# Performance work log

Hardware: AMD Instinct MI355X
Metric: run time of the kernel (lower is better)

Reference implementation:

```python
import jax, jax.numpy as jnp
from jax import lax
import numpy as np

KSIZE = 3
STRIDE = 1
PAD = 1
SOFTMAX_SCALE = 10.0
EPS = 1e-4


def _unfold(x, k, stride, pad):
    # x: [B, C, H, W] -> ([B, L, C, k, k], Ho, Wo)  (matches torch nn.Unfold ordering)
    B, C, H, W = x.shape
    xp = jnp.pad(x, ((0, 0), (0, 0), (pad, pad), (pad, pad)))
    Ho = (H + 2 * pad - k) // stride + 1
    Wo = (W + 2 * pad - k) // stride + 1
    cols = jnp.stack(
        [xp[:, :, i:i + Ho * stride:stride, j:j + Wo * stride:stride]
         for i in range(k) for j in range(k)], axis=2)  # [B, C, k*k, Ho, Wo]
    cols = cols.reshape(B, C, k, k, Ho * Wo)
    return cols.transpose(0, 4, 1, 2, 3), Ho, Wo


def setup_inputs() -> dict:
    key = jax.random.key(0)
    kb, kf, km = jax.random.split(key, 3)
    b = jax.random.normal(kb, (4, 64, 64, 64), dtype=jnp.float32)
    f = jax.random.normal(kf, (4, 64, 64, 64), dtype=jnp.float32)
    mask = jax.random.uniform(km, (4, 1, 256, 256), dtype=jnp.float32)
    return {"b": b, "f": f, "mask": mask}


def reference(b, f, mask):
    B, C, H, W = f.shape
    k = KSIZE
    # background patches: [B, L, C, k, k]
    bp, _, _ = _unfold(b, k, STRIDE, PAD)
    # mask: avg_pool2d(kernel=4, stride=mask_scale) with mask_scale = mask.W // f.W = 4
    mp = mask.reshape(B, 1, H, 4, W, 4).mean(axis=(3, 5))  # [B, 1, H, W]
    m_unf, _, _ = _unfold(mp, k, STRIDE, PAD)  # [B, L, 1, k, k]
    m0 = m_unf[0]  # quirk of original code: first sample's mask patches used for all
    w = bp * m0[None]  # masked background patches [B, L, C, k, k]
    f_masked = f * (1.0 - mp)
    # L2 norm over (C, k, k) per patch
    norm = jnp.sqrt(jnp.sum(w * w, axis=(2, 3, 4), keepdims=True) + EPS)
    wn = w / norm
    # cosine-similarity score: conv2d(f_masked, wn) as a GEMM over unfolded f
    fp, Ho, Wo = _unfold(f_masked, k, STRIDE, PAD)  # [B, Q, C, k, k]
    score = jnp.einsum('bqcij,blcij->blq', fp, wn).reshape(B, -1, Ho, Wo)  # [B, L, Ho, Wo]
    attn = jax.nn.softmax(score * SOFTMAX_SCALE, axis=1)
    offsets = jnp.argmax(score, axis=1)[:, None]  # [B, 1, Ho, Wo]
    # conv_transpose2d(attn, w, padding=1) == conv2d with spatially flipped, channel-swapped kernel
    pad_ct = k - 1 - 1

    def _ct(a, w_i):  # a: [L, Ho, Wo], w_i: [L, C, k, k]
        kern = jnp.flip(w_i, axis=(-2, -1)).transpose(1, 0, 2, 3)  # [C, L, k, k]
        return lax.conv_general_dilated(
            a[None], kern, (1, 1), [(pad_ct, pad_ct), (pad_ct, pad_ct)],
            dimension_numbers=('NCHW', 'OIHW', 'NCHW'))[0]

    y = jax.vmap(_ct)(attn, w)  # [B, C, Ho, Wo]
    return y, offsets
```

## Files before the change

### kernel.cpp

```cpp
#include <hip/hip_runtime.h>
#include <math.h>

typedef unsigned int u32;
typedef unsigned short u16;
typedef unsigned long long u64;
typedef _Float16 h8v __attribute__((ext_vector_type(8)));
typedef float f4v __attribute__((ext_vector_type(4)));
typedef u32 u4v __attribute__((ext_vector_type(4)));

#define B_ 4
#define C_ 64
#define HW 4096
#define L_ 4096
#define D_ 576
#define MW 256
#define SCALE 10.0f
#define EPS 1e-4f
#define TAU 0.015f
#define PAIRCAP 262144

__device__ __forceinline__ u16 f16b(float x) {
  union { _Float16 h; u16 u; } c; c.h = (_Float16)x; return c.u;
}
__device__ __forceinline__ float f16f(u16 v) {
  union { u16 u; _Float16 h; } c; c.u = v; return (float)c.h;
}

__device__ __forceinline__ void gld16(const void* g, void* l) {
  __builtin_amdgcn_global_load_lds((const __attribute__((address_space(1))) void*)g,
                                   (__attribute__((address_space(3))) void*)l, 16, 0, 0);
}

__global__ __launch_bounds__(256) void k_mp(const float* __restrict__ mask, float* __restrict__ mp) {
  int idx = blockIdx.x * 256 + threadIdx.x;
  int b = idx >> 12, p = idx & 4095;
  int y = p >> 6, x = p & 63;
  const float* mb = mask + (size_t)b * MW * MW;
  float s = 0.f;
  #pragma unroll
  for (int i = 0; i < 4; ++i)
    #pragma unroll
    for (int j = 0; j < 4; ++j)
      s += mb[(y * 4 + i) * MW + x * 4 + j];
  mp[idx] = s * (1.f / 16.f);
}

__global__ __launch_bounds__(256) void k_pre2(const float* __restrict__ f, const float* __restrict__ mp,
                                              float* __restrict__ m0, float* __restrict__ fm) {
  int blk = blockIdx.x;
  if (blk < 144) {
    int idx = blk * 256 + threadIdx.x;
    int l = idx / 9, t = idx - l * 9;
    int ly = l >> 6, lx = l & 63;
    int i = t / 3, j = t - i * 3;
    int yy = ly + i - 1, xx = lx + j - 1;
    float v = 0.f;
    if ((unsigned)yy < 64u && (unsigned)xx < 64u) v = mp[(yy << 6) + xx];
    m0[idx] = v;
  } else {
    int idx = (blk - 144) * 256 + threadIdx.x;
    int p = idx & 4095;
    int b = idx >> 18;
    fm[idx] = f[idx] * (1.f - mp[(b << 12) + p]);
  }
}

__device__ __forceinline__ float ldsval(const float* __restrict__ s, int lloc, int c, int t) {
  int i2 = t / 3, j2 = t - i2 * 3;
  int xx = lloc + j2 - 1;
  float v = 0.f;
  if ((unsigned)xx < 64u) v = s[(((i2 << 6) + c) << 6) + xx];
  return v;
}

__global__ __launch_bounds__(512) void k_prepw(const float* __restrict__ bimg, const float* __restrict__ fmb,
                                               const float* __restrict__ m0,
                                               u16* __restrict__ w_h, u16* __restrict__ fp_h,
                                               u16* __restrict__ wT_h,
                                               double* __restrict__ norme, float* __restrict__ normv,
                                               int* __restrict__ rcount, int* __restrict__ pcount,
                                               u64* __restrict__ rbest) {
  if (blockIdx.x >= 64) {
    int e = (blockIdx.x - 64) * 512 + threadIdx.x;
    if (e < 4096) rbest[e] = 0ull;
    if (e == 0) { *rcount = 0; *pcount = 0; }
    return;
  }
  __shared__ float s_img[12288];
  __shared__ float s_fm[12288];
  __shared__ float m0s[576];
  const int ly = blockIdx.x;
  const int tid = threadIdx.x;

  #pragma unroll
  for (int i = 0; i < 6; ++i) {
    int slot = tid + i * 512;
    int dy = slot >> 10, rem = slot & 1023;
    int c = rem >> 4, xq = rem & 15;
    int yy = ly + dy - 1;
    f4v vi = {0.f, 0.f, 0.f, 0.f}, vf = {0.f, 0.f, 0.f, 0.f};
    if ((unsigned)yy < 64u) {
      vi = *(const f4v*)&bimg[(c << 12) + (yy << 6) + (xq << 2)];
      vf = *(const f4v*)&fmb[(c << 12) + (yy << 6) + (xq << 2)];
    }
    *(f4v*)&s_img[slot << 2] = vi;
    *(f4v*)&s_fm[slot << 2] = vf;
  }
  for (int t2 = tid; t2 < 576; t2 += 512) m0s[t2] = m0[ly * 576 + t2];
  __syncthreads();

  u32* wh32 = (u32*)w_h;
  u32* fp32p = (u32*)fp_h;
  #pragma unroll
  for (int i = 0; i < 36; ++i) {
    int g2 = tid + i * 512;
    int idx = g2 * 2;
    int ll = idx / 576, d0 = idx - ll * 576;
    int c0 = d0 / 9, t0 = d0 - c0 * 9;
    int d1 = d0 + 1;
    int c1 = d1 / 9, t1 = d1 - c1 * 9;
    float w0 = ldsval(s_img, ll, c0, t0) * m0s[ll * 9 + t0];
    float w1 = ldsval(s_img, ll, c1, t1) * m0s[ll * 9 + t1];
    wh32[ly * 18432 + g2] = (u32)f16b(w0) | ((u32)f16b(w1) << 16);
    float p0 = ldsval(s_fm, ll, c0, t0);
    float p1 = ldsval(s_fm, ll, c1, t1);
    fp32p[ly * 18432 + g2] = (u32)f16b(p0) | ((u32)f16b(p1) << 16);
  }

  u32* wT32 = (u32*)wT_h;
  #pragma unroll
  for (int i = 0; i < 36; ++i) {
    int g2 = tid + i * 512;
    int d = g2 >> 5, lxp = g2 & 31;
    int c = d / 9, t = d - c * 9;
    float w0 = ldsval(s_img, 2 * lxp, c, t) * m0s[(2 * lxp) * 9 + t];
    float w1 = ldsval(s_img, 2 * lxp + 1, c, t) * m0s[(2 * lxp + 1) * 9 + t];
    wT32[d * 2048 + ly * 32 + lxp] = (u32)f16b(w0) | ((u32)f16b(w1) << 16);
  }

  int wid = tid >> 6, lane = tid & 63;
  #pragma unroll
  for (int it = 0; it < 8; ++it) {
    int lloc = wid * 8 + it;
    double ss = 0.0;
    #pragma unroll
    for (int k = 0; k < 9; ++k) {
      int d = lane + k * 64;
      int c = d / 9, t = d - c * 9;
      float wv = ldsval(s_img, lloc, c, t) * m0s[lloc * 9 + t];
      ss += (double)wv * (double)wv;
    }
    #pragma unroll
    for (int off = 32; off; off >>= 1) ss += __shfl_down(ss, off);
    if (lane == 0) {
      double n = sqrt(ss + (double)EPS);
      norme[ly * 64 + lloc] = n;
      normv[ly * 64 + lloc] = (float)n;
    }
  }
}

#define STAGE1(buf, k0) do {                                                             \
    int bb = (buf) * 24576;                                                              \
    _Pragma("unroll") for (int i_ = 0; i_ < 4; ++i_) {                                   \
      int s_ = tid + i_ * 256; int r_ = s_ >> 2, ks_ = s_ & 3;                           \
      int kg_ = ks_ ^ ((r_ >> 1) & 3);                                                   \
      gld16(A + (u32)(m0 + r_) * 576u + (u32)((k0) + kg_ * 8),                           \
            (char*)lds + bb + s_ * 16); }                                                \
    _Pragma("unroll") for (int i_ = 0; i_ < 2; ++i_) {                                   \
      int s_ = tid + i_ * 256; int r_ = s_ >> 2, ks_ = s_ & 3;                           \
      int kg_ = ks_ ^ ((r_ >> 1) & 3);                                                   \
      gld16(Bm + (u32)(n0 + r_) * 576u + (u32)((k0) + kg_ * 8),                          \
            (char*)lds + bb + 16384 + s_ * 16); }                                        \
  } while (0)

__global__ __launch_bounds__(256, 2) void k_mfma1(
    const u16* __restrict__ A, const u16* __restrict__ Bm, const float* __restrict__ normv,
    u16* __restrict__ P, float* __restrict__ bm1, int* __restrict__ bi1,
    float* __restrict__ bsum, int* __restrict__ bflg)
{
  __shared__ u32 lds[18432];
  u16* ldsu = (u16*)lds;
  const int tid = threadIdx.x;
  const int lane = tid & 63, wid = tid >> 6;
  const int wrM = wid >> 1, wc = wid & 1;
  const int kq = lane >> 4, li = lane & 15;

  int nwg = gridDim.x * gridDim.y;
  int bid = blockIdx.y * gridDim.x + blockIdx.x;
  int cpx = nwg >> 3;
  int swz = (bid & 7) * cpx + (bid >> 3);
  int bx = swz % gridDim.x, by = swz / gridDim.x;
  const int m0 = by * 256, n0 = bx * 128;

  f4v acc[8][4] = {};

  STAGE1(0, 0);
  STAGE1(1, 32);

  for (int kc = 0; kc < 18; ++kc) {
    if (kc + 1 < 18) { asm volatile("s_waitcnt vmcnt(6)" ::: "memory"); }
    else             { asm volatile("s_waitcnt vmcnt(0)" ::: "memory"); }
    __builtin_amdgcn_s_barrier();
    __builtin_amdgcn_sched_barrier(0);
    if (kc + 2 < 18) STAGE1((kc + 2) % 3, (kc + 2) * 32);

    int cb = (kc % 3) * 12288;
    h8v ah[8];
    #pragma unroll
    for (int mf = 0; mf < 8; ++mf) {
      int r = wrM * 128 + mf * 16 + li;
      int off = r * 32 + (kq ^ ((r >> 1) & 3)) * 8;
      ah[mf] = *(const h8v*)&ldsu[cb + off];
    }
    #pragma unroll
    for (int nf = 0; nf < 4; ++nf) {
      int r = wc * 64 + nf * 16 + li;
      int off = r * 32 + (kq ^ ((r >> 1) & 3)) * 8;
      h8v bh = *(const h8v*)&ldsu[cb + 8192 + off];
      #pragma unroll
      for (int mf = 0; mf < 8; ++mf)
        acc[mf][nf] = __builtin_amdgcn_mfma_f32_16x16x32_f16(ah[mf], bh, acc[mf][nf], 0, 0, 0);
    }
  }
  __syncthreads();

  float* ldsf = (float*)lds;
  int*   ldsi = (int*)lds;

  float invn4[4];
  #pragma unroll
  for (int nf = 0; nf < 4; ++nf) invn4[nf] = 1.0f / normv[n0 + wc * 64 + nf * 16 + li];
  #pragma unroll
  for (int mf = 0; mf < 8; ++mf)
    #pragma unroll
    for (int nf = 0; nf < 4; ++nf)
      #pragma unroll
      for (int rr = 0; rr < 4; ++rr)
        acc[mf][nf][rr] *= invn4[nf];

  #pragma unroll
  for (int mf = 0; mf < 8; ++mf)
    #pragma unroll
    for (int rr = 0; rr < 4; ++rr) {
      int row = wrM * 128 + mf * 16 + kq * 4 + rr;
      float tv = fmaxf(fmaxf(acc[mf][0][rr], acc[mf][1][rr]), fmaxf(acc[mf][2][rr], acc[mf][3][rr]));
      ldsf[row * 33 + wc * 16 + li] = tv;
    }
  __syncthreads();
  float rV1 = -3.4e38f;
  #pragma unroll
  for (int k = 0; k < 32; ++k) rV1 = fmaxf(rV1, ldsf[tid * 33 + k]);
  ldsf[8448 + tid] = rV1;
  ldsi[8704 + tid] = 0x7fffffff;
  ldsi[8960 + tid] = 0;
  __syncthreads();

  #pragma unroll
  for (int mf = 0; mf < 8; ++mf)
    #pragma unroll
    for (int rr = 0; rr < 4; ++rr) {
      int row = wrM * 128 + mf * 16 + kq * 4 + rr;
      float v1 = ldsf[8448 + row];
      int m = m0 + row;
      float sum4 = 0.f;
      int locmin = 0x7fffffff, loccnt = 0;
      #pragma unroll
      for (int nf = 0; nf < 4; ++nf) {
        float sv = acc[mf][nf][rr];
        int n = n0 + wc * 64 + nf * 16 + li;
        float p = __expf((sv - v1) * SCALE);
        P[(u32)m * 4096u + (u32)n] = f16b(p);
        sum4 += p;
        if (sv == v1 && n < locmin) locmin = n;
        if (sv >= v1 - TAU) loccnt++;
      }
      ldsf[row * 33 + wc * 16 + li] = sum4;
      if (locmin != 0x7fffffff) atomicMin(&ldsi[8704 + row], locmin);
      if (loccnt) atomicAdd(&ldsi[8960 + row], loccnt);
    }
  __syncthreads();

  {
    float rS = 0.f;
    #pragma unroll
    for (int k = 0; k < 32; ++k) rS += ldsf[tid * 33 + k];
    int q = m0 + tid, j = n0 >> 7;
    bm1[q * 32 + j] = ldsf[8448 + tid];
    bi1[q * 32 + j] = ldsi[8704 + tid];
    bsum[q * 32 + j] = rS;
    bflg[q * 32 + j] = (ldsi[8960 + tid] >= 2) ? 1 : 0;
  }
}

__global__ __launch_bounds__(256) void k_smred(const float* __restrict__ bm1, const int* __restrict__ bi1,
                                               const float* __restrict__ bsum, const int* __restrict__ bflg,
                                               float* __restrict__ fac, float* __restrict__ gm,
                                               float* __restrict__ offs, int* __restrict__ rflag,
                                               int* __restrict__ rlist, int* __restrict__ rcount) {
  int q = blockIdx.x * 4 + (threadIdx.x >> 6);
  int lane = threadIdx.x & 63;
  if (lane >= 32) return;
  float mj = bm1[q * 32 + lane];
  int   fj = bflg[q * 32 + lane];
  float v1 = mj; int i1 = bi1[q * 32 + lane];
  #pragma unroll
  for (int d = 1; d < 32; d <<= 1) {
    float ov1 = __shfl_xor(v1, d); int oi1 = __shfl_xor(i1, d);
    if (ov1 > v1 || (ov1 == v1 && oi1 < i1)) { v1 = ov1; i1 = oi1; }
  }
  float e = __expf((mj - v1) * SCALE);
  float Z = bsum[q * 32 + lane] * e;
  #pragma unroll
  for (int d = 1; d < 32; d <<= 1) Z += __shfl_xor(Z, d);
  fac[q * 32 + lane] = e / Z;
  int jwin = i1 >> 7;
  int near = (lane != jwin) && (mj >= v1 - TAU);
  u64 bal = __ballot(near);
  int wflg = __shfl(fj, jwin);
  if (lane == 0) {
    gm[q] = v1;
    offs[q] = (float)i1;
    int fl = (bal != 0ull || wflg) ? 1 : 0;
    rflag[q] = fl;
    if (fl) {
      int pos = atomicAdd(rcount, 1);
      if (pos < 4096) rlist[pos] = q;
    }
  }
}

__global__ __launch_bounds__(256) void k_attnc(u16* __restrict__ P, const float* __restrict__ fac,
                                               const int* __restrict__ rflag, const float* __restrict__ bm1,
                                               const float* __restrict__ gm,
                                               u32* __restrict__ pairs, int* __restrict__ pcount) {
  int gid = blockIdx.x * 256 + threadIdx.x;
  u4v v = ((u4v*)P)[gid];
  int q = gid >> 9;
  int l0 = (gid & 511) * 8;
  int j = l0 >> 7;

  if (rflag[q]) {
    float thr = gm[q] - 2.0f * TAU - 1e-3f;
    float bmj = bm1[q * 32 + j];
    if (bmj >= thr) {
      u16 bits = f16b(__expf((thr - bmj) * SCALE));
      u16 pt = bits > 4 ? (u16)(bits - 4) : (u16)1;
      #pragma unroll
      for (int k = 0; k < 4; ++k) {
        u16 lo = (u16)v[k], hi = (u16)(v[k] >> 16);
        if (lo >= pt) {
          int pos = atomicAdd(pcount, 1);
          if (pos < PAIRCAP) pairs[pos] = ((u32)q << 12) | (u32)(l0 + 2 * k);
        }
        if (hi >= pt) {
          int pos = atomicAdd(pcount, 1);
          if (pos < PAIRCAP) pairs[pos] = ((u32)q << 12) | (u32)(l0 + 2 * k + 1);
        }
      }
    }
  }

  _Float16 fh = (_Float16)fac[q * 32 + j];
  union { u4v u; h8v h; } c; c.u = v;
  c.h *= (h8v){fh, fh, fh, fh, fh, fh, fh, fh};
  ((u4v*)P)[gid] = c.u;
}

#define STG2(buf, k0) do {                                                               \
    int bb = (buf) * 24576;                                                              \
    _Pragma("unroll") for (int i_ = 0; i_ < 4; ++i_) {                                   \
      int s_ = tid + i_ * 256; int r_ = s_ >> 2, ks_ = s_ & 3;                           \
      int kg_ = ks_ ^ ((r_ >> 1) & 3);                                                   \
      gld16(A + (u32)(m0 + r_) * 4096u + (u32)((k0) + kg_ * 8),                          \
            (char*)lds + bb + s_ * 16); }                                                \
    _Pragma("unroll") for (int i_ = 0; i_ < 2; ++i_) {                                   \
      int s_ = tid + i_ * 256; int r_ = s_ >> 2, ks_ = s_ & 3;                           \
      int kg_ = ks_ ^ ((r_ >> 1) & 3);                                                   \
      gld16(Bm + (u32)(n0 + r_) * 4096u + (u32)((k0) + kg_ * 8),                         \
            (char*)lds + bb + 16384 + s_ * 16); }                                        \
  } while (0)

__global__ __launch_bounds__(256, 2) void k_gemm2(
    const u16* __restrict__ A, const u16* __restrict__ Bm, float* __restrict__ Gpart)
{
  __shared__ u32 lds[18432];
  u16* ldsu = (u16*)lds;
  const int tid = threadIdx.x;
  const int lane = tid & 63, wid = tid >> 6;
  const int wrM = wid >> 1, wc = wid & 1;
  const int kq = lane >> 4, li = lane & 15;

  int nwg = gridDim.x * gridDim.y;
  int bid = blockIdx.y * gridDim.x + blockIdx.x;
  int cpx = nwg >> 3;
  int swz = (bid & 7) * cpx + (bid >> 3);
  int bx = swz % gridDim.x, by = swz / gridDim.x;
  const int m0 = by * 256, n0 = bx * 128;
  const int kz = blockIdx.z * 1024;

  f4v acc[8][4] = {};

  STG2(0, kz);
  STG2(1, kz + 32);

  for (int kc = 0; kc < 32; ++kc) {
    if (kc + 1 < 32) { asm volatile("s_waitcnt vmcnt(6)" ::: "memory"); }
    else             { asm volatile("s_waitcnt vmcnt(0)" ::: "memory"); }
    __builtin_amdgcn_s_barrier();
    __builtin_amdgcn_sched_barrier(0);
    if (kc + 2 < 32) STG2((kc + 2) % 3, kz + (kc + 2) * 32);

    int cb = (kc % 3) * 12288;
    h8v ah[8];
    #pragma unroll
    for (int mf = 0; mf < 8; ++mf) {
      int r = wrM * 128 + mf * 16 + li;
      int off = r * 32 + (kq ^ ((r >> 1) & 3)) * 8;
      ah[mf] = *(const h8v*)&ldsu[cb + off];
    }
    #pragma unroll
    for (int nf = 0; nf < 4; ++nf) {
      int r = wc * 64 + nf * 16 + li;
      int off = r * 32 + (kq ^ ((r >> 1) & 3)) * 8;
      h8v bh = *(const h8v*)&ldsu[cb + 8192 + off];
      #pragma unroll
      for (int mf = 0; mf < 8; ++mf)
        acc[mf][nf] = __builtin_amdgcn_mfma_f32_16x16x32_f16(ah[mf], bh, acc[mf][nf], 0, 0, 0);
    }
  }

  float* Cf = Gpart + (size_t)blockIdx.z * 2359296;
  #pragma unroll
  for (int nf = 0; nf < 4; ++nf) {
    int n = n0 + wc * 64 + nf * 16 + li;
    if (n < D_) {
      #pragma unroll
      for (int mf = 0; mf < 8; ++mf) {
        int m = m0 + wrM * 128 + mf * 16 + kq * 4;
        *(f4v*)&Cf[(u32)n * 4096u + (u32)m] = acc[mf][nf];
      }
    }
  }
}

__global__ __launch_bounds__(256) void k_rpairs(const u32* __restrict__ pairs, const int* __restrict__ pcount,
                                                const float* __restrict__ b0, const float* __restrict__ m0,
                                                const float* __restrict__ fmb, const double* __restrict__ norme,
                                                u64* __restrict__ rbest) {
  int nw = gridDim.x * 4;
  int gw = blockIdx.x * 4 + (threadIdx.x >> 6);
  int lane = threadIdx.x & 63;
  int cnt = *pcount; if (cnt > PAIRCAP) cnt = PAIRCAP;
  for (int e = gw; e < cnt; e += nw) {
    u32 pr = pairs[e];
    int q = pr >> 12, l = pr & 4095;
    int qy = q >> 6, qx = q & 63, ly = l >> 6, lx = l & 63;
    int c = lane;
    double dot = 0.0;
    #pragma unroll
    for (int t = 0; t < 9; ++t) {
      int i = t / 3, j = t - (t / 3) * 3;
      int wy = ly + i - 1, wx = lx + j - 1;
      int fy = qy + i - 1, fx = qx + j - 1;
      float wv = 0.f, fv = 0.f;
      if ((unsigned)wy < 64u && (unsigned)wx < 64u) wv = b0[(c << 12) + (wy << 6) + wx] * m0[l * 9 + t];
      if ((unsigned)fy < 64u && (unsigned)fx < 64u) fv = fmb[(c << 12) + (fy << 6) + fx];
      dot += (double)wv * (double)fv;
    }
    #pragma unroll
    for (int off = 32; off; off >>= 1) dot += __shfl_down(dot, off);
    if (lane == 0) {
      double sc = dot / norme[l];
      u64 bbits = (u64)__double_as_longlong(sc);
      if (bbits >> 63) bbits = ~bbits; else bbits |= 0x8000000000000000ull;
      u64 key = (bbits & ~0xFFFull) | (u64)(4095 - l);
      atomicMax(rbest + q, key);
    }
  }
}

__global__ __launch_bounds__(256) void k_foldfin(const float* __restrict__ Gp, float* __restrict__ yout,
                                                 const int* __restrict__ rlist, const int* __restrict__ rcount,
                                                 const u64* __restrict__ rbest, float* __restrict__ offs) {
  if (blockIdx.x < 1024) {
    int idx = blockIdx.x * 256 + threadIdx.x;
    int c = idx >> 12, p = idx & 4095;
    int yy = p >> 6, xx = p & 63;
    float s = 0.f;
    #pragma unroll
    for (int t = 0; t < 9; ++t) {
      int i = t / 3, j = t - (t / 3) * 3;
      int qy = yy + 1 - i, qx = xx + 1 - j;
      if ((unsigned)qy < 64u && (unsigned)qx < 64u) {
        u32 base = (u32)(c * 9 + t) * 4096u + (u32)((qy << 6) + qx);
        #pragma unroll
        for (int z = 0; z < 4; ++z) s += Gp[(size_t)z * 2359296 + base];
      }
    }
    yout[idx] = s;
  } else {
    int cnt = *rcount; if (cnt > 4096) cnt = 4096;
    int e = (blockIdx.x - 1024) * 256 + threadIdx.x;
    if (e < cnt) {
      int q = rlist[e];
      offs[q] = (float)(4095 - (int)(rbest[q] & 0xFFFull));
    }
  }
}

extern "C" void kernel_launch(void* const* d_in, const int* in_sizes, int n_in,
                              void* d_out, int out_size, void* d_ws, size_t ws_size,
                              hipStream_t stream) {
  const float* b_in = (const float*)d_in[0];
  const float* f_in = (const float*)d_in[1];
  const float* mask = (const float*)d_in[2];
  float* out = (float*)d_out;

  char* ws = (char*)d_ws;
  float*  mp     = (float*)(ws + 0);
  float*  m0buf  = (float*)(ws + 65536);
  float*  fm     = (float*)(ws + 212992);
  float*  normv  = (float*)(ws + 4407296);
  double* norme  = (double*)(ws + 4423680);
  u16*    w_h    = (u16*)(ws + 4456448);
  u16*    fp_h   = (u16*)(ws + 9175040);
  u16*    wT_h   = (u16*)(ws + 13893632);
  u16*    P      = (u16*)(ws + 19136512);
  int*    rflag  = (int*)(ws + 52690944);
  float*  bm1    = (float*)(ws + 86245376);
  int*    bi1    = (int*)(ws + 86769664);
  float*  bsum   = (float*)(ws + 87293952);
  int*    bflg   = (int*)(ws + 87818240);
  float*  fac    = (float*)(ws + 88342528);
  float*  gm     = (float*)(ws + 88866816);
  float*  Gpart  = (float*)(ws + 88883200);
  int*    rcount = (int*)(ws + 126631936);
  int*    pcount = (int*)(ws + 126631940);
  int*    rlist  = (int*)(ws + 126632192);
  u64*    rbest  = (u64*)(ws + 126648576);
  u32*    pairs  = (u32*)(ws + 126681344);

  k_mp<<<64, 256, 0, stream>>>(mask, mp);
  k_pre2<<<4240, 256, 0, stream>>>(f_in, mp, m0buf, fm);

  for (int b = 0; b < B_; ++b) {
    const float* bimg = b_in + (size_t)b * C_ * HW;
    const float* fmb  = fm + (size_t)b * C_ * HW;
    float* offs_b = out + (size_t)B_ * C_ * HW + (size_t)b * HW;

    k_prepw<<<80, 512, 0, stream>>>(bimg, fmb, m0buf, w_h, fp_h, wT_h,
                                    norme, normv, rcount, pcount, rbest);
    k_mfma1<<<dim3(32, 16), 256, 0, stream>>>(fp_h, w_h, normv, P, bm1, bi1, bsum, bflg);
    k_smred<<<1024, 256, 0, stream>>>(bm1, bi1, bsum, bflg, fac, gm, offs_b, rflag, rlist, rcount);
    k_attnc<<<8192, 256, 0, stream>>>(P, fac, rflag, bm1, gm, pairs, pcount);
    k_gemm2<<<dim3(5, 16, 4), 256, 0, stream>>>(P, wT_h, Gpart);
    k_rpairs<<<512, 256, 0, stream>>>(pairs, pcount, bimg, m0buf, fmb, norme, rbest);
    k_foldfin<<<1040, 256, 0, stream>>>(Gpart, out + (size_t)b * C_ * HW,
                                        rlist, rcount, rbest, offs_b);
  }
}
```

Measured before the change: 584.2 us.

## Load GEMM operands directly from global into registers, dropping LDS staging

Both MFMA GEMM kernels stop staging A/B tiles through a triple-buffered LDS pipeline fed by global_load_lds, and instead have each lane load its fragments straight from global memory into registers every k-step. This removes LDS traffic, barriers and waitcnt synchronisation, and shrinks LDS use in the first kernel. The cost is that the data reuse LDS provided across waves is lost: each wave re-fetches overlapping rows from global/L2. It also loses explicit prefetch overlap, leaving latency hiding to the compiler and to occupancy.

```diff
diff --git a/kernel.cpp b/kernel.cpp
--- a/kernel.cpp
+++ b/kernel.cpp
@@ -24,11 +24,6 @@
 }
 __device__ __forceinline__ float f16f(u16 v) {
   union { u16 u; _Float16 h; } c; c.u = v; return (float)c.h;
-}
-
-__device__ __forceinline__ void gld16(const void* g, void* l) {
-  __builtin_amdgcn_global_load_lds((const __attribute__((address_space(1))) void*)g,
-                                   (__attribute__((address_space(3))) void*)l, 16, 0, 0);
 }
 
 __global__ __launch_bounds__(256) void k_mp(const float* __restrict__ mask, float* __restrict__ mp) {
@@ -160,27 +155,12 @@
   }
 }
 
-#define STAGE1(buf, k0) do {                                                             \
-    int bb = (buf) * 24576;                                                              \
-    _Pragma("unroll") for (int i_ = 0; i_ < 4; ++i_) {                                   \
-      int s_ = tid + i_ * 256; int r_ = s_ >> 2, ks_ = s_ & 3;                           \
-      int kg_ = ks_ ^ ((r_ >> 1) & 3);                                                   \
-      gld16(A + (u32)(m0 + r_) * 576u + (u32)((k0) + kg_ * 8),                           \
-            (char*)lds + bb + s_ * 16); }                                                \
-    _Pragma("unroll") for (int i_ = 0; i_ < 2; ++i_) {                                   \
-      int s_ = tid + i_ * 256; int r_ = s_ >> 2, ks_ = s_ & 3;                           \
-      int kg_ = ks_ ^ ((r_ >> 1) & 3);                                                   \
-      gld16(Bm + (u32)(n0 + r_) * 576u + (u32)((k0) + kg_ * 8),                          \
-            (char*)lds + bb + 16384 + s_ * 16); }                                        \
-  } while (0)
-
 __global__ __launch_bounds__(256, 2) void k_mfma1(
     const u16* __restrict__ A, const u16* __restrict__ Bm, const float* __restrict__ normv,
     u16* __restrict__ P, float* __restrict__ bm1, int* __restrict__ bi1,
     float* __restrict__ bsum, int* __restrict__ bflg)
 {
-  __shared__ u32 lds[18432];
-  u16* ldsu = (u16*)lds;
+  __shared__ u32 lds[9472];
   const int tid = threadIdx.x;
   const int lane = tid & 63, wid = tid >> 6;
   const int wrM = wid >> 1, wc = wid & 1;
@@ -195,35 +175,24 @@
 
   f4v acc[8][4] = {};
 
-  STAGE1(0, 0);
-  STAGE1(1, 32);
-
+  const u32 aoff = (u32)(m0 + wrM * 128 + li) * 576u + (u32)(kq * 8);
+  const u32 boff = (u32)(n0 + wc * 64 + li) * 576u + (u32)(kq * 8);
+
+  #pragma unroll 2
   for (int kc = 0; kc < 18; ++kc) {
-    if (kc + 1 < 18) { asm volatile("s_waitcnt vmcnt(6)" ::: "memory"); }
-    else             { asm volatile("s_waitcnt vmcnt(0)" ::: "memory"); }
-    __builtin_amdgcn_s_barrier();
-    __builtin_amdgcn_sched_barrier(0);
-    if (kc + 2 < 18) STAGE1((kc + 2) % 3, (kc + 2) * 32);
-
-    int cb = (kc % 3) * 12288;
-    h8v ah[8];
-    #pragma unroll
-    for (int mf = 0; mf < 8; ++mf) {
-      int r = wrM * 128 + mf * 16 + li;
-      int off = r * 32 + (kq ^ ((r >> 1) & 3)) * 8;
-      ah[mf] = *(const h8v*)&ldsu[cb + off];
-    }
-    #pragma unroll
-    for (int nf = 0; nf < 4; ++nf) {
-      int r = wc * 64 + nf * 16 + li;
-      int off = r * 32 + (kq ^ ((r >> 1) & 3)) * 8;
-      h8v bh = *(const h8v*)&ldsu[cb + 8192 + off];
+    h8v af[8], bf[4];
+    #pragma unroll
+    for (int mf = 0; mf < 8; ++mf)
+      af[mf] = *(const h8v*)(A + aoff + (u32)(mf * 9216) + (u32)(kc * 32));
+    #pragma unroll
+    for (int nf = 0; nf < 4; ++nf)
+      bf[nf] = *(const h8v*)(Bm + boff + (u32)(nf * 9216) + (u32)(kc * 32));
+    #pragma unroll
+    for (int nf = 0; nf < 4; ++nf)
       #pragma unroll
       for (int mf = 0; mf < 8; ++mf)
-        acc[mf][nf] = __builtin_amdgcn_mfma_f32_16x16x32_f16(ah[mf], bh, acc[mf][nf], 0, 0, 0);
-    }
-  }
-  __syncthreads();
+        acc[mf][nf] = __builtin_amdgcn_mfma_f32_16x16x32_f16(af[mf], bf[nf], acc[mf][nf], 0, 0, 0);
+  }
 
   float* ldsf = (float*)lds;
   int*   ldsi = (int*)lds;
@@ -367,25 +336,9 @@
   ((u4v*)P)[gid] = c.u;
 }
 
-#define STG2(buf, k0) do {                                                               \
-    int bb = (buf) * 24576;                                                              \
-    _Pragma("unroll") for (int i_ = 0; i_ < 4; ++i_) {                                   \
-      int s_ = tid + i_ * 256; int r_ = s_ >> 2, ks_ = s_ & 3;                           \
-      int kg_ = ks_ ^ ((r_ >> 1) & 3);                                                   \
-      gld16(A + (u32)(m0 + r_) * 4096u + (u32)((k0) + kg_ * 8),                          \
-            (char*)lds + bb + s_ * 16); }                                                \
-    _Pragma("unroll") for (int i_ = 0; i_ < 2; ++i_) {                                   \
-      int s_ = tid + i_ * 256; int r_ = s_ >> 2, ks_ = s_ & 3;                           \
-      int kg_ = ks_ ^ ((r_ >> 1) & 3);                                                   \
-      gld16(Bm + (u32)(n0 + r_) * 4096u + (u32)((k0) + kg_ * 8),                         \
-            (char*)lds + bb + 16384 + s_ * 16); }                                        \
-  } while (0)
-
 __global__ __launch_bounds__(256, 2) void k_gemm2(
     const u16* __restrict__ A, const u16* __restrict__ Bm, float* __restrict__ Gpart)
 {
-  __shared__ u32 lds[18432];
-  u16* ldsu = (u16*)lds;
   const int tid = threadIdx.x;
   const int lane = tid & 63, wid = tid >> 6;
   const int wrM = wid >> 1, wc = wid & 1;
@@ -397,37 +350,27 @@
   int swz = (bid & 7) * cpx + (bid >> 3);
   int bx = swz % gridDim.x, by = swz / gridDim.x;
   const int m0 = by * 256, n0 = bx * 128;
-  const int kz = blockIdx.z * 1024;
+  const u32 kz = (u32)blockIdx.z * 1024u;
 
   f4v acc[8][4] = {};
 
-  STG2(0, kz);
-  STG2(1, kz + 32);
-
+  const u32 aoff = (u32)(m0 + wrM * 128 + li) * 4096u + kz + (u32)(kq * 8);
+  const u32 boff = (u32)(n0 + wc * 64 + li) * 4096u + kz + (u32)(kq * 8);
+
+  #pragma unroll 2
   for (int kc = 0; kc < 32; ++kc) {
-    if (kc + 1 < 32) { asm volatile("s_waitcnt vmcnt(6)" ::: "memory"); }
-    else             { asm volatile("s_waitcnt vmcnt(0)" ::: "memory"); }
-    __builtin_amdgcn_s_barrier();
-    __builtin_amdgcn_sched_barrier(0);
-    if (kc + 2 < 32) STG2((kc + 2) % 3, kz + (kc + 2) * 32);
-
-    int cb = (kc % 3) * 12288;
-    h8v ah[8];
-    #pragma unroll
-    for (int mf = 0; mf < 8; ++mf) {
-      int r = wrM * 128 + mf * 16 + li;
-      int off = r * 32 + (kq ^ ((r >> 1) & 3)) * 8;
-      ah[mf] = *(const h8v*)&ldsu[cb + off];
-    }
-    #pragma unroll
-    for (int nf = 0; nf < 4; ++nf) {
-      int r = wc * 64 + nf * 16 + li;
-      int off = r * 32 + (kq ^ ((r >> 1) & 3)) * 8;
-      h8v bh = *(const h8v*)&ldsu[cb + 8192 + off];
+    h8v af[8], bf[4];
+    #pragma unroll
+    for (int mf = 0; mf < 8; ++mf)
+      af[mf] = *(const h8v*)(A + aoff + (u32)(mf * 65536) + (u32)(kc * 32));
+    #pragma unroll
+    for (int nf = 0; nf < 4; ++nf)
+      bf[nf] = *(const h8v*)(Bm + boff + (u32)(nf * 65536) + (u32)(kc * 32));
+    #pragma unroll
+    for (int nf = 0; nf < 4; ++nf)
       #pragma unroll
       for (int mf = 0; mf < 8; ++mf)
-        acc[mf][nf] = __builtin_amdgcn_mfma_f32_16x16x32_f16(ah[mf], bh, acc[mf][nf], 0, 0, 0);
-    }
+        acc[mf][nf] = __builtin_amdgcn_mfma_f32_16x16x32_f16(af[mf], bf[nf], acc[mf][nf], 0, 0, 0);
   }
 
   float* Cf = Gpart + (size_t)blockIdx.z * 2359296;
```

After: 934.3 us. 1.6x slower.
